# Performance work log

Hardware: AMD Instinct MI355X
Metric: run time of the kernel (lower is better)

## Reference

```python
import jax, jax.numpy as jnp
import numpy as np

LMAX, RB, RA, N, D = 4, 12, 11, 131072, 64
S = (LMAX + 1) ** 2


def _assoc_legendre_norm(lmax, x):
    # Fully-normalized associated Legendre P_l^m(x), orthonormal over the sphere
    # (includes sqrt((2l+1)/(4pi) * (l-m)!/(l+m)!)). x: [B] = cos(beta).
    B = x.shape[0]
    s = np.sqrt(np.clip(1.0 - x * x, 0.0, 1.0))
    P = np.zeros((lmax + 1, lmax + 1, B))
    P[0, 0] = np.sqrt(1.0 / (4.0 * np.pi))
    for m in range(1, lmax + 1):
        P[m, m] = -np.sqrt((2.0 * m + 1.0) / (2.0 * m)) * s * P[m - 1, m - 1]
    for m in range(0, lmax):
        P[m + 1, m] = np.sqrt(2.0 * m + 3.0) * x * P[m, m]
    for m in range(0, lmax + 1):
        for l in range(m + 2, lmax + 1):
            a = np.sqrt((4.0 * l * l - 1.0) / (l * l - m * m))
            b = np.sqrt((((l - 1) ** 2 - m * m)) / (4.0 * (l - 1) ** 2 - 1.0))
            P[l, m] = a * (x * P[l - 1, m] - b * P[l - 2, m])
    return P


def _sh_grid(lmax, res_beta, res_alpha):
    # Real orthonormal spherical harmonics sampled on a Gauss-Legendre x uniform-alpha grid,
    # plus quadrature weights so that sum_{b,a} Y_i Y_j qw_b = delta_ij (band-limited).
    x, w = np.polynomial.legendre.leggauss(res_beta)  # nodes in cos(beta)
    alpha = 2.0 * np.pi * np.arange(res_alpha) / res_alpha
    P = _assoc_legendre_norm(lmax, x)  # [L+1, L+1, RB]
    Ssz = (lmax + 1) ** 2
    Y = np.zeros((res_beta, res_alpha, Ssz))
    i = 0
    for l in range(lmax + 1):
        for m in range(-l, l + 1):
            if m < 0:
                ang = np.sqrt(2.0) * np.sin(-m * alpha)
            elif m == 0:
                ang = np.ones_like(alpha)
            else:
                ang = np.sqrt(2.0) * np.cos(m * alpha)
            Y[:, :, i] = P[l, abs(m)][:, None] * ang[None, :]
            i += 1
    qw = w * (2.0 * np.pi / res_alpha)  # beta quadrature * alpha trapezoid weight
    return Y.astype(np.float32), qw.astype(np.float32)


def setup_inputs() -> dict:
    key = jax.random.key(0)
    k1, k2, k3, k4 = jax.random.split(key, 4)
    Y_np, qw_np = _sh_grid(LMAX, RB, RA)
    Y = jnp.asarray(Y_np)                       # [RB, RA, S]
    Yw = Y * jnp.asarray(qw_np)[:, None, None]  # [RB, RA, S] (quadrature-weighted)
    input1 = jax.random.normal(k1, (N, D), dtype=jnp.float32)
    input2 = jax.random.normal(k2, (N, D), dtype=jnp.float32)
    W1 = jax.random.normal(k3, (D, S), dtype=jnp.float32) * 0.1
    W2 = jax.random.normal(k4, (D, S), dtype=jnp.float32) * 0.1
    return {"input1": input1, "input2": input2, "W1": W1, "W2": W2, "Y": Y, "Yw": Yw}


def reference(input1, input2, W1, W2, Y, Yw):
    # linear_in: project input irreps to S2 spherical-harmonic coefficients
    c1 = input1 @ W1  # [N, S]
    c2 = input2 @ W2  # [N, S]
    # ToS2Grid: evaluate band-limited signal on the (beta, alpha) grid
    g1 = jnp.einsum("ns,bas->nba", c1, Y)  # [N, RB, RA]
    g2 = jnp.einsum("ns,bas->nba", c2, Y)
    # pointwise product on the sphere, then FromS2Grid (quadrature projection)
    return jnp.einsum("nba,bas->ns", g1 * g2, Yw)  # [N, S]
```

## Files before the change

### kernel.cpp

```cpp
#include <hip/hip_runtime.h>


typedef _Float16 f16x8 __attribute__((ext_vector_type(8)));
typedef _Float16 f16x4 __attribute__((ext_vector_type(4)));
typedef float f32x4 __attribute__((ext_vector_type(4)));
typedef float f32x4u __attribute__((ext_vector_type(4), aligned(4)));

namespace {
constexpr int kD = 64, kS = 25, kP = 132;
constexpr int kBlock = 256, kM = 64;
constexpr int kYfOff = 0;
constexpr int kYwOff = 4608;
constexpr int kWfOff = 9216;
constexpr int kWsHalfs = 13312;
}

__global__ void precompute11(const float* __restrict__ W1,
                             const float* __restrict__ W2,
                             const float* __restrict__ Y,
                             const float* __restrict__ Yw,
                             _Float16* __restrict__ ws) {
    const int e = blockIdx.x * blockDim.x + threadIdx.x;
    if (e < 4608) {
        const int i = e & 3, ln = (e >> 2) & 63, r = e >> 8;
        const int pt = r >> 1, st = r & 1;
        const int p = pt * 16 + (ln & 15);
        const int s = st * 16 + ((ln >> 4) & 3) * 4 + i;
        ws[kYfOff + e] = (s < kS && p < kP) ? (_Float16)Y[p * kS + s]
                                            : (_Float16)0.f;
    } else if (e < 9216) {
        const int e2 = e - 4608;
        const int i = e2 & 3, ln = (e2 >> 2) & 63, r = e2 >> 8;
        const int pt = r % 9, st = r / 9;
        const int p = pt * 16 + ((ln >> 4) & 3) * 4 + i;
        const int s = st * 16 + (ln & 15);
        ws[kYwOff + e2] = (s < kS && p < kP) ? (_Float16)Yw[p * kS + s]
                                             : (_Float16)0.f;
    } else if (e < kWsHalfs) {
        const int e3 = e - 9216;
        const int j = e3 & 7, ln = (e3 >> 3) & 63, r = e3 >> 9;
        const int ks = r & 1, st = (r >> 1) & 1, op = r >> 2;
        const int s = st * 16 + (ln & 15);
        const int d = ks * 32 + ((ln >> 4) & 3) * 8 + j;
        const float* W = op ? W2 : W1;
        ws[kWfOff + e3] = (s < kS) ? (_Float16)W[d * kS + s] : (_Float16)0.f;
    }
}

__device__ __forceinline__ f16x8 ld8(const _Float16* p) {
    return *reinterpret_cast<const f16x8*>(p);
}
__device__ __forceinline__ f16x4 ld4(const _Float16* p) {
    return *reinterpret_cast<const f16x4*>(p);
}
__device__ __forceinline__ f16x8 cvt8h(f32x4 u, f32x4 v) {
    f16x8 r;
    r[0] = (_Float16)u[0]; r[1] = (_Float16)u[1];
    r[2] = (_Float16)u[2]; r[3] = (_Float16)u[3];
    r[4] = (_Float16)v[0]; r[5] = (_Float16)v[1];
    r[6] = (_Float16)v[2]; r[7] = (_Float16)v[3];
    return r;
}

__global__ __launch_bounds__(kBlock, 4) void gaunt_fused11(
    const float* __restrict__ in1, const float* __restrict__ in2,
    const _Float16* __restrict__ ws, float* __restrict__ out)
{
    __shared__ f32x4 ldsq[2][kM][16];

    const int tid  = threadIdx.x;
    const int lane = tid & 63;
    const int w    = __builtin_amdgcn_readfirstlane(tid >> 6);
    const int lo16 = lane & 15, quad = lane >> 4;

    const long long rowbase = (long long)blockIdx.x * kM;

    {
        const int rg = lane >> 4;
        const int sl = lane & 15;
        #pragma unroll
        for (int i = 0; i < 8; ++i) {
            const int t  = w * 8 + i;
            const int op = t >> 4, q = t & 15;
            const int r  = q * 4 + rg;
            const int c16 = sl ^ (r & 7);
            const float* src = (op ? in2 : in1) + (rowbase + r) * kD + c16 * 4;
            char* dst = (char*)(&ldsq[0][0][0]) + op * 16384 + q * 1024;
            __builtin_amdgcn_global_load_lds(
                (const __attribute__((address_space(1))) void*)src,
                (__attribute__((address_space(3))) void*)dst,
                16, 0, 0);
        }
    }

    const _Float16* wsYf = ws + kYfOff;
    const _Float16* wsYw = ws + kYwOff;
    const _Float16* wsWf = ws + kWfOff;

    f16x8 w1f[2][2], w2f[2][2];
    #pragma unroll
    for (int st = 0; st < 2; ++st)
        #pragma unroll
        for (int ks = 0; ks < 2; ++ks) {
            w1f[st][ks] = ld8(&wsWf[((0 * 2 + st) * 2 + ks) * 512 + lane * 8]);
            w2f[st][ks] = ld8(&wsWf[((1 * 2 + st) * 2 + ks) * 512 + lane * 8]);
        }
    f16x4 yfc0 = ld4(&wsYf[0 * 256 + lane * 4]);
    f16x4 yfc1 = ld4(&wsYf[1 * 256 + lane * 4]);
    f16x4 yw0c = ld4(&wsYw[0 * 256 + lane * 4]);
    f16x4 yw1c = ld4(&wsYw[9 * 256 + lane * 4]);

    __syncthreads();

    const int r  = w * 16 + lo16;
    const int r7 = lo16 & 7;
    f16x8 b1[2], b2[2];
    #pragma unroll
    for (int ks = 0; ks < 2; ++ks) {
        const int s0 = ks * 8 + quad * 2;
        const f32x4 u = ldsq[0][r][s0 ^ r7];
        const f32x4 v = ldsq[0][r][(s0 + 1) ^ r7];
        b1[ks] = cvt8h(u, v);
    }
    #pragma unroll
    for (int ks = 0; ks < 2; ++ks) {
        const int s0 = ks * 8 + quad * 2;
        const f32x4 u = ldsq[1][r][s0 ^ r7];
        const f32x4 v = ldsq[1][r][(s0 + 1) ^ r7];
        b2[ks] = cvt8h(u, v);
    }

    f16x4 h1c[2], h2c[2];
    #pragma unroll
    for (int st = 0; st < 2; ++st) {
        f32x4 c1 = (f32x4){0.f, 0.f, 0.f, 0.f};
        f32x4 c2 = (f32x4){0.f, 0.f, 0.f, 0.f};
        #pragma unroll
        for (int ks = 0; ks < 2; ++ks) {
            c1 = __builtin_amdgcn_mfma_f32_16x16x32_f16(w1f[st][ks], b1[ks], c1, 0, 0, 0);
            c2 = __builtin_amdgcn_mfma_f32_16x16x32_f16(w2f[st][ks], b2[ks], c2, 0, 0, 0);
        }
        #pragma unroll
        for (int i = 0; i < 4; ++i) {
            h1c[st][i] = (_Float16)c1[i];
            h2c[st][i] = (_Float16)c2[i];
        }
    }

    f32x4 oacc0 = (f32x4){0.f, 0.f, 0.f, 0.f};
    f32x4 oacc1 = (f32x4){0.f, 0.f, 0.f, 0.f};

    #pragma unroll 1
    for (int pt = 0; pt < 9; ++pt) {
        f16x4 yfn0, yfn1, yw0n, yw1n;
        if (pt < 8) {
            yfn0 = ld4(&wsYf[((pt + 1) * 2 + 0) * 256 + lane * 4]);
            yfn1 = ld4(&wsYf[((pt + 1) * 2 + 1) * 256 + lane * 4]);
            yw0n = ld4(&wsYw[(0 * 9 + pt + 1) * 256 + lane * 4]);
            yw1n = ld4(&wsYw[(1 * 9 + pt + 1) * 256 + lane * 4]);
        }
        const f32x4 z = (f32x4){0.f, 0.f, 0.f, 0.f};
        f32x4 g1 = __builtin_amdgcn_mfma_f32_16x16x16f16(yfc0, h1c[0], z, 0, 0, 0);
        g1       = __builtin_amdgcn_mfma_f32_16x16x16f16(yfc1, h1c[1], g1, 0, 0, 0);
        f32x4 g2 = __builtin_amdgcn_mfma_f32_16x16x16f16(yfc0, h2c[0], z, 0, 0, 0);
        g2       = __builtin_amdgcn_mfma_f32_16x16x16f16(yfc1, h2c[1], g2, 0, 0, 0);
        f16x4 h;
        h[0] = (_Float16)(g1[0] * g2[0]);
        h[1] = (_Float16)(g1[1] * g2[1]);
        h[2] = (_Float16)(g1[2] * g2[2]);
        h[3] = (_Float16)(g1[3] * g2[3]);
        oacc0 = __builtin_amdgcn_mfma_f32_16x16x16f16(yw0c, h, oacc0, 0, 0, 0);
        oacc1 = __builtin_amdgcn_mfma_f32_16x16x16f16(yw1c, h, oacc1, 0, 0, 0);
        yfc0 = yfn0; yfc1 = yfn1; yw0c = yw0n; yw1c = yw1n;
    }

    float* rp = out + (rowbase + r) * kS;
    *reinterpret_cast<f32x4u*>(rp + quad * 4) = oacc0;
    if (quad < 2) {
        *reinterpret_cast<f32x4u*>(rp + 16 + quad * 4) = oacc1;
    } else if (quad == 2) {
        rp[24] = oacc1[0];
    }
}

extern "C" void kernel_launch(void* const* d_in, const int* in_sizes, int n_in,
                              void* d_out, int out_size, void* d_ws, size_t ws_size,
                              hipStream_t stream) {
    const float* in1 = (const float*)d_in[0];
    const float* in2 = (const float*)d_in[1];
    const float* W1  = (const float*)d_in[2];
    const float* W2  = (const float*)d_in[3];
    const float* Y   = (const float*)d_in[4];
    const float* Yw  = (const float*)d_in[5];
    float* out = (float*)d_out;
    _Float16* ws = (_Float16*)d_ws;

    precompute11<<<52, 256, 0, stream>>>(W1, W2, Y, Yw, ws);

    const int n_rows = in_sizes[0] / kD;
    const int grid = n_rows / kM;
    gaunt_fused11<<<grid, kBlock, 0, stream>>>(in1, in2, ws, out);
}
```

Measured before the change: 112.6 us.

## Process four row chunks per block with double-buffered async LDS staging

Each block now handles four 64-row chunks instead of one. Input rows are staged into two LDS buffers with async global-to-LDS loads, so the next chunk's load overlaps the current chunk's MFMA work, with vmcnt waits and barriers between stages. All Y/Yw/W fragments are loaded once into registers per block and reused across chunks, which cuts their per-block reload cost. In exchange register pressure rises (launch bounds drop to 2 blocks per SIMD-set), LDS doubles, and the grid shrinks to a quarter of its size, which may reduce latency hiding through occupancy.

```diff
diff --git a/kernel.cpp b/kernel.cpp
--- a/kernel.cpp
+++ b/kernel.cpp
@@ -8,14 +8,16 @@
 
 namespace {
 constexpr int kD = 64, kS = 25, kP = 132;
-constexpr int kBlock = 256, kM = 64;
+constexpr int kBlock = 256;
+constexpr int kCh = 64;
+constexpr int kChunks = 4;
 constexpr int kYfOff = 0;
 constexpr int kYwOff = 4608;
 constexpr int kWfOff = 9216;
 constexpr int kWsHalfs = 13312;
 }
 
-__global__ void precompute11(const float* __restrict__ W1,
+__global__ void precompute12(const float* __restrict__ W1,
                              const float* __restrict__ W2,
                              const float* __restrict__ Y,
                              const float* __restrict__ Yw,
@@ -62,124 +64,145 @@
     return r;
 }
 
-__global__ __launch_bounds__(kBlock, 4) void gaunt_fused11(
+__global__ __launch_bounds__(kBlock, 2) void gaunt_fused12(
     const float* __restrict__ in1, const float* __restrict__ in2,
     const _Float16* __restrict__ ws, float* __restrict__ out)
 {
-    __shared__ f32x4 ldsq[2][kM][16];
+    __shared__ f32x4 ldsq[2][2][kCh][16];
 
     const int tid  = threadIdx.x;
     const int lane = tid & 63;
     const int w    = __builtin_amdgcn_readfirstlane(tid >> 6);
     const int lo16 = lane & 15, quad = lane >> 4;
-
-    const long long rowbase = (long long)blockIdx.x * kM;
-
-    {
-        const int rg = lane >> 4;
-        const int sl = lane & 15;
+    const long long rowbase = (long long)blockIdx.x * (kChunks * kCh);
+
+    const int rg = lane >> 4;
+    const int sl = lane & 15;
+
+    auto stage = [&](int chunk, int buf) {
         #pragma unroll
         for (int i = 0; i < 8; ++i) {
             const int t  = w * 8 + i;
             const int op = t >> 4, q = t & 15;
             const int r  = q * 4 + rg;
             const int c16 = sl ^ (r & 7);
-            const float* src = (op ? in2 : in1) + (rowbase + r) * kD + c16 * 4;
-            char* dst = (char*)(&ldsq[0][0][0]) + op * 16384 + q * 1024;
+            const float* src = (op ? in2 : in1)
+                + (rowbase + chunk * kCh + r) * kD + c16 * 4;
+            char* dst = (char*)(&ldsq[buf][op][q * 4][0]);
             __builtin_amdgcn_global_load_lds(
                 (const __attribute__((address_space(1))) void*)src,
                 (__attribute__((address_space(3))) void*)dst,
                 16, 0, 0);
         }
-    }
+    };
+
+    stage(0, 0);
 
     const _Float16* wsYf = ws + kYfOff;
     const _Float16* wsYw = ws + kYwOff;
     const _Float16* wsWf = ws + kWfOff;
 
-    f16x8 w1f[2][2], w2f[2][2];
-    #pragma unroll
-    for (int st = 0; st < 2; ++st)
-        #pragma unroll
-        for (int ks = 0; ks < 2; ++ks) {
-            w1f[st][ks] = ld8(&wsWf[((0 * 2 + st) * 2 + ks) * 512 + lane * 8]);
-            w2f[st][ks] = ld8(&wsWf[((1 * 2 + st) * 2 + ks) * 512 + lane * 8]);
-        }
-    f16x4 yfc0 = ld4(&wsYf[0 * 256 + lane * 4]);
-    f16x4 yfc1 = ld4(&wsYf[1 * 256 + lane * 4]);
-    f16x4 yw0c = ld4(&wsYw[0 * 256 + lane * 4]);
-    f16x4 yw1c = ld4(&wsYw[9 * 256 + lane * 4]);
-
-    __syncthreads();
+    f16x8 wf[2][2][2];
+    #pragma unroll
+    for (int op = 0; op < 2; ++op)
+        #pragma unroll
+        for (int st = 0; st < 2; ++st)
+            #pragma unroll
+            for (int ks = 0; ks < 2; ++ks)
+                wf[op][st][ks] = ld8(&wsWf[((op * 2 + st) * 2 + ks) * 512 + lane * 8]);
+
+    f16x4 yf[9][2], yw[2][9];
+    #pragma unroll
+    for (int pt = 0; pt < 9; ++pt) {
+        yf[pt][0] = ld4(&wsYf[(pt * 2 + 0) * 256 + lane * 4]);
+        yf[pt][1] = ld4(&wsYf[(pt * 2 + 1) * 256 + lane * 4]);
+        yw[0][pt] = ld4(&wsYw[(0 * 9 + pt) * 256 + lane * 4]);
+        yw[1][pt] = ld4(&wsYw[(1 * 9 + pt) * 256 + lane * 4]);
+    }
+
+    stage(1, 1);
 
     const int r  = w * 16 + lo16;
     const int r7 = lo16 & 7;
-    f16x8 b1[2], b2[2];
-    #pragma unroll
-    for (int ks = 0; ks < 2; ++ks) {
-        const int s0 = ks * 8 + quad * 2;
-        const f32x4 u = ldsq[0][r][s0 ^ r7];
-        const f32x4 v = ldsq[0][r][(s0 + 1) ^ r7];
-        b1[ks] = cvt8h(u, v);
-    }
-    #pragma unroll
-    for (int ks = 0; ks < 2; ++ks) {
-        const int s0 = ks * 8 + quad * 2;
-        const f32x4 u = ldsq[1][r][s0 ^ r7];
-        const f32x4 v = ldsq[1][r][(s0 + 1) ^ r7];
-        b2[ks] = cvt8h(u, v);
-    }
-
-    f16x4 h1c[2], h2c[2];
-    #pragma unroll
-    for (int st = 0; st < 2; ++st) {
-        f32x4 c1 = (f32x4){0.f, 0.f, 0.f, 0.f};
-        f32x4 c2 = (f32x4){0.f, 0.f, 0.f, 0.f};
-        #pragma unroll
-        for (int ks = 0; ks < 2; ++ks) {
-            c1 = __builtin_amdgcn_mfma_f32_16x16x32_f16(w1f[st][ks], b1[ks], c1, 0, 0, 0);
-            c2 = __builtin_amdgcn_mfma_f32_16x16x32_f16(w2f[st][ks], b2[ks], c2, 0, 0, 0);
-        }
-        #pragma unroll
-        for (int i = 0; i < 4; ++i) {
-            h1c[st][i] = (_Float16)c1[i];
-            h2c[st][i] = (_Float16)c2[i];
-        }
-    }
-
-    f32x4 oacc0 = (f32x4){0.f, 0.f, 0.f, 0.f};
-    f32x4 oacc1 = (f32x4){0.f, 0.f, 0.f, 0.f};
-
-    #pragma unroll 1
-    for (int pt = 0; pt < 9; ++pt) {
-        f16x4 yfn0, yfn1, yw0n, yw1n;
-        if (pt < 8) {
-            yfn0 = ld4(&wsYf[((pt + 1) * 2 + 0) * 256 + lane * 4]);
-            yfn1 = ld4(&wsYf[((pt + 1) * 2 + 1) * 256 + lane * 4]);
-            yw0n = ld4(&wsYw[(0 * 9 + pt + 1) * 256 + lane * 4]);
-            yw1n = ld4(&wsYw[(1 * 9 + pt + 1) * 256 + lane * 4]);
-        }
-        const f32x4 z = (f32x4){0.f, 0.f, 0.f, 0.f};
-        f32x4 g1 = __builtin_amdgcn_mfma_f32_16x16x16f16(yfc0, h1c[0], z, 0, 0, 0);
-        g1       = __builtin_amdgcn_mfma_f32_16x16x16f16(yfc1, h1c[1], g1, 0, 0, 0);
-        f32x4 g2 = __builtin_amdgcn_mfma_f32_16x16x16f16(yfc0, h2c[0], z, 0, 0, 0);
-        g2       = __builtin_amdgcn_mfma_f32_16x16x16f16(yfc1, h2c[1], g2, 0, 0, 0);
-        f16x4 h;
-        h[0] = (_Float16)(g1[0] * g2[0]);
-        h[1] = (_Float16)(g1[1] * g2[1]);
-        h[2] = (_Float16)(g1[2] * g2[2]);
-        h[3] = (_Float16)(g1[3] * g2[3]);
-        oacc0 = __builtin_amdgcn_mfma_f32_16x16x16f16(yw0c, h, oacc0, 0, 0, 0);
-        oacc1 = __builtin_amdgcn_mfma_f32_16x16x16f16(yw1c, h, oacc1, 0, 0, 0);
-        yfc0 = yfn0; yfc1 = yfn1; yw0c = yw0n; yw1c = yw1n;
-    }
-
-    float* rp = out + (rowbase + r) * kS;
-    *reinterpret_cast<f32x4u*>(rp + quad * 4) = oacc0;
-    if (quad < 2) {
-        *reinterpret_cast<f32x4u*>(rp + 16 + quad * 4) = oacc1;
-    } else if (quad == 2) {
-        rp[24] = oacc1[0];
+
+    f32x4 o0[kChunks], o1[kChunks];
+    #pragma unroll
+    for (int c = 0; c < kChunks; ++c) {
+        o0[c] = (f32x4){0.f, 0.f, 0.f, 0.f};
+        o1[c] = (f32x4){0.f, 0.f, 0.f, 0.f};
+    }
+
+    auto compute = [&](int buf, f32x4& o0c, f32x4& o1c) {
+        f16x8 b[2][2];
+        #pragma unroll
+        for (int op = 0; op < 2; ++op)
+            #pragma unroll
+            for (int ks = 0; ks < 2; ++ks) {
+                const int s0 = ks * 8 + quad * 2;
+                const f32x4 u = ldsq[buf][op][r][s0 ^ r7];
+                const f32x4 v = ldsq[buf][op][r][(s0 + 1) ^ r7];
+                b[op][ks] = cvt8h(u, v);
+            }
+        f16x4 h1[2], h2[2];
+        #pragma unroll
+        for (int st = 0; st < 2; ++st) {
+            f32x4 c1 = (f32x4){0.f, 0.f, 0.f, 0.f};
+            f32x4 c2 = (f32x4){0.f, 0.f, 0.f, 0.f};
+            #pragma unroll
+            for (int ks = 0; ks < 2; ++ks) {
+                c1 = __builtin_amdgcn_mfma_f32_16x16x32_f16(wf[0][st][ks], b[0][ks], c1, 0, 0, 0);
+                c2 = __builtin_amdgcn_mfma_f32_16x16x32_f16(wf[1][st][ks], b[1][ks], c2, 0, 0, 0);
+            }
+            #pragma unroll
+            for (int i = 0; i < 4; ++i) {
+                h1[st][i] = (_Float16)c1[i];
+                h2[st][i] = (_Float16)c2[i];
+            }
+        }
+        #pragma unroll
+        for (int pt = 0; pt < 9; ++pt) {
+            const f32x4 z = (f32x4){0.f, 0.f, 0.f, 0.f};
+            f32x4 g1 = __builtin_amdgcn_mfma_f32_16x16x16f16(yf[pt][0], h1[0], z, 0, 0, 0);
+            g1       = __builtin_amdgcn_mfma_f32_16x16x16f16(yf[pt][1], h1[1], g1, 0, 0, 0);
+            f32x4 g2 = __builtin_amdgcn_mfma_f32_16x16x16f16(yf[pt][0], h2[0], z, 0, 0, 0);
+            g2       = __builtin_amdgcn_mfma_f32_16x16x16f16(yf[pt][1], h2[1], g2, 0, 0, 0);
+            f16x4 h;
+            h[0] = (_Float16)(g1[0] * g2[0]);
+            h[1] = (_Float16)(g1[1] * g2[1]);
+            h[2] = (_Float16)(g1[2] * g2[2]);
+            h[3] = (_Float16)(g1[3] * g2[3]);
+            o0c = __builtin_amdgcn_mfma_f32_16x16x16f16(yw[0][pt], h, o0c, 0, 0, 0);
+            o1c = __builtin_amdgcn_mfma_f32_16x16x16f16(yw[1][pt], h, o1c, 0, 0, 0);
+        }
+    };
+
+    asm volatile("s_waitcnt vmcnt(8)" ::: "memory");
+    __builtin_amdgcn_s_barrier();
+    compute(0, o0[0], o1[0]);
+    __builtin_amdgcn_s_barrier();
+    stage(2, 0);
+    asm volatile("s_waitcnt vmcnt(8)" ::: "memory");
+    __builtin_amdgcn_s_barrier();
+    compute(1, o0[1], o1[1]);
+    __builtin_amdgcn_s_barrier();
+    stage(3, 1);
+    asm volatile("s_waitcnt vmcnt(8)" ::: "memory");
+    __builtin_amdgcn_s_barrier();
+    compute(0, o0[2], o1[2]);
+    asm volatile("s_waitcnt vmcnt(0)" ::: "memory");
+    __builtin_amdgcn_s_barrier();
+    compute(1, o0[3], o1[3]);
+
+    #pragma unroll
+    for (int c = 0; c < kChunks; ++c) {
+        const long long row = rowbase + c * kCh + r;
+        float* rp = out + row * kS;
+        *reinterpret_cast<f32x4u*>(rp + quad * 4) = o0[c];
+        if (quad < 2) {
+            *reinterpret_cast<f32x4u*>(rp + 16 + quad * 4) = o1[c];
+        } else if (quad == 2) {
+            rp[24] = o1[c][0];
+        }
     }
 }
 
@@ -195,9 +218,9 @@
     float* out = (float*)d_out;
     _Float16* ws = (_Float16*)d_ws;
 
-    precompute11<<<52, 256, 0, stream>>>(W1, W2, Y, Yw, ws);
+    precompute12<<<52, 256, 0, stream>>>(W1, W2, Y, Yw, ws);
 
     const int n_rows = in_sizes[0] / kD;
-    const int grid = n_rows / kM;
-    gaunt_fused11<<<grid, kBlock, 0, stream>>>(in1, in2, ws, out);
-}
+    const int grid = n_rows / (kChunks * kCh);
+    gaunt_fused12<<<grid, kBlock, 0, stream>>>(in1, in2, ws, out);
+}
```

Result: faster. 108.0 us (-4.1%).
